# Kernel tuning notes

Measured on AMD Instinct MI355X. Metric: run time of the kernel, lower is better.

Reference implementation:

```python
import jax, jax.numpy as jnp
import numpy as np

N_NODES = 100000


def setup_inputs() -> dict:
    key = jax.random.key(0)
    ks = jax.random.split(key, 10)
    N, T, IN, H, OUT = N_NODES, 20, 1, 64, 1
    E = 3200000
    s = 1.0 / np.sqrt(H)
    return {
        "x": jax.random.normal(ks[0], (N, T, IN), dtype=jnp.float32),
        "edge_index": jax.random.randint(ks[1], (E, 2), 0, N, dtype=jnp.int64),
        "W_ih": jax.random.uniform(ks[2], (H, IN), jnp.float32, -s, s),
        "b_ih": jax.random.uniform(ks[3], (H,), jnp.float32, -s, s),
        "W_hh": jax.random.uniform(ks[4], (H, H), jnp.float32, -s, s),
        "b_hh": jax.random.uniform(ks[5], (H,), jnp.float32, -s, s),
        "W_gcn": jax.random.uniform(ks[6], (H, H), jnp.float32, -s, s),
        "b_gcn": jax.random.uniform(ks[7], (H,), jnp.float32, -s, s),
        "W_fc": jax.random.uniform(ks[8], (OUT, H), jnp.float32, -s, s),
        "b_fc": jax.random.uniform(ks[9], (OUT,), jnp.float32, -s, s),
    }


def _strnn_fwd(x, edge_index, W_ih, b_ih, W_hh, b_hh, W_gcn, b_gcn, W_fc, b_fc):
    N = x.shape[0]
    H = W_hh.shape[0]

    # ---- vanilla tanh RNN (batch_first); only last hidden state is needed ----
    xs = jnp.swapaxes(x, 0, 1)  # [T, N, in]

    def step(h, xt):
        h = jnp.tanh(xt @ W_ih.T + b_ih + h @ W_hh.T + b_hh)
        return h, None

    h_last, _ = jax.lax.scan(step, jnp.zeros((N, H), x.dtype), xs)  # [N, H]

    # ---- GCNConv: add self-loops, sym-normalize, linear, scatter-add ----
    src = edge_index[:, 0]
    dst = edge_index[:, 1]
    loop = jnp.arange(N, dtype=src.dtype)
    src = jnp.concatenate([src, loop])
    dst = jnp.concatenate([dst, loop])

    xw = h_last @ W_gcn.T  # [N, H]
    deg = jax.ops.segment_sum(jnp.ones_like(dst, dtype=xw.dtype), dst, num_segments=N)
    dinv = jnp.where(deg > 0, jax.lax.rsqrt(deg), 0.0)
    norm = dinv[src] * dinv[dst]  # [E+N]

    msgs = xw[src] * norm[:, None]  # gather + scale, [E+N, H]
    agg = jax.ops.segment_sum(msgs, dst, num_segments=N) + b_gcn  # scatter-add

    return agg @ W_fc.T + b_fc  # [N, out]


def reference(x, edge_index, W_ih, b_ih, W_hh, b_hh, W_gcn, b_gcn, W_fc, b_fc):
    return _strnn_fwd(x, edge_index, W_ih, b_ih, W_hh, b_hh, W_gcn, b_gcn, W_fc, b_fc)
```

## Files before the change

kernel.cpp:

```cpp
#include <hip/hip_runtime.h>

#define TT 20
#define HH 64
#define RSZ 32768
#define DRSZ 16384
#define NSL 64
#define NSLD 32

typedef __attribute__((ext_vector_type(8))) short short8;
typedef __attribute__((ext_vector_type(4))) float f32x4;

__device__ __forceinline__ unsigned fbits(float f) { union { float f; unsigned u; } v; v.f = f; return v.u; }
__device__ __forceinline__ float bcast(unsigned u) { union { float f; unsigned u; } v; v.u = u; return v.f; }

__global__ __launch_bounds__(256, 3) void k_fused(
    const float* __restrict__ x,
    const float* __restrict__ W_ih, const float* __restrict__ b_ih,
    const float* __restrict__ W_hh, const float* __restrict__ b_hh,
    const float* __restrict__ W_gcn, const float* __restrict__ W_fc,
    const int* __restrict__ ei, unsigned* __restrict__ degrep,
    float* __restrict__ z, int N, int E, int RD, int N2)
{
    __shared__ __align__(16) unsigned smem[8192];

    const int t = threadIdx.x;
    const int RDN = RD * NSLD;

    if (blockIdx.x < RDN) {
        unsigned* bin = smem;
        const int r = blockIdx.x % RD;
        const int s = blockIdx.x / RD;
        const int base = r * DRSZ;
        for (int i = t; i < DRSZ / 2; i += 256) bin[i] = 0;
        __syncthreads();
        const long long P = (long long)(E >> 1);
        const long long pb = s * P / NSLD;
        const long long pe = (s + 1) * P / NSLD;
        const int4* ei4 = (const int4*)ei;
        for (long long g = pb + t; g < pe; g += 256) {
            int4 q = ei4[g];
            unsigned u0 = (unsigned)(q.y - base);
            unsigned u1 = (unsigned)(q.w - base);
            if (u0 < DRSZ) atomicAdd(&bin[u0 >> 1], 1u << ((u0 & 1) << 4));
            if (u1 < DRSZ) atomicAdd(&bin[u1 >> 1], 1u << ((u1 & 1) << 4));
        }
        if ((E & 1) && s == NSLD - 1 && t == 0) {
            unsigned u = (unsigned)(ei[2 * (E - 1) + 1] - base);
            if (u < DRSZ) atomicAdd(&bin[u >> 1], 1u << ((u & 1) << 4));
        }
        __syncthreads();
        const int lim = min(DRSZ, N - base);
        const int words = (lim + 1) >> 1;
        unsigned* dst = degrep + (size_t)s * N2 + (base >> 1);
        for (int i = t; i < words; i += 256) dst[i] = bin[i];
        return;
    }

    const int w    = t >> 6;
    const int l    = t & 63;
    const int nl   = l & 15;
    const int quad = l >> 4;
    const int n0   = (blockIdx.x - RDN) * 64 + w * 16;

    unsigned short* hh = (unsigned short*)&smem[w * 512];
    unsigned short* hl = (unsigned short*)&smem[2048 + w * 512];
    float*          sx = (float*)&smem[4096 + w * 320];

    for (int i = l; i < 16 * TT; i += 64) {
        int nn = i / TT, tt = i - nn * TT;
        int n = n0 + nn; if (n >= N) n = N - 1;
        sx[tt * 16 + nn] = x[(size_t)n * TT + tt];
    }
    {
        uint4 zz = {0, 0, 0, 0};
        uint4* ph = (uint4*)hh;
        uint4* pl = (uint4*)hl;
#pragma unroll
        for (int i = 0; i < 2; ++i) { ph[l + 64 * i] = zz; pl[l + 64 * i] = zz; }
    }

    short8 Bh[4][2], Bl[4][2];
#pragma unroll
    for (int tt2 = 0; tt2 < 4; ++tt2)
#pragma unroll
        for (int kc = 0; kc < 2; ++kc) {
            const float* wr = W_hh + (size_t)(16 * tt2 + nl) * HH + kc * 32 + quad * 8;
            float4 w0 = *(const float4*)(wr);
            float4 w1 = *(const float4*)(wr + 4);
            float wvv[8] = {w0.x, w0.y, w0.z, w0.w, w1.x, w1.y, w1.z, w1.w};
            short8 sh, sl;
#pragma unroll
            for (int j = 0; j < 8; ++j) {
                unsigned u  = fbits(wvv[j]);
                unsigned hb = u & 0xffff0000u;
                float lo = wvv[j] - bcast(hb);
                sh[j] = (short)(hb >> 16);
                sl[j] = (short)(fbits(lo) >> 16);
            }
            Bh[tt2][kc] = sh; Bl[tt2][kc] = sl;
        }

    float vl = 0.0f;
#pragma unroll 8
    for (int j = 0; j < HH; ++j) vl = fmaf(W_fc[j], W_gcn[j * HH + l], vl);

    float wih4[4], bs4[4], vv[4];
#pragma unroll
    for (int tt2 = 0; tt2 < 4; ++tt2) {
        int n = nl + 16 * tt2;
        wih4[tt2] = W_ih[n];
        bs4[tt2]  = b_ih[n] + b_hh[n];
        vv[tt2]   = __shfl(vl, n, 64);
    }

    const int ra = (l ^ ((l >> 4) & 1)) * 8;

    f32x4 C[4];

    for (int step = 0; step < TT; ++step) {
        const float4 xr = *(const float4*)&sx[step * 16 + quad * 4];
#pragma unroll
        for (int tt2 = 0; tt2 < 4; ++tt2) {
            C[tt2][0] = fmaf(xr.x, wih4[tt2], bs4[tt2]);
            C[tt2][1] = fmaf(xr.y, wih4[tt2], bs4[tt2]);
            C[tt2][2] = fmaf(xr.z, wih4[tt2], bs4[tt2]);
            C[tt2][3] = fmaf(xr.w, wih4[tt2], bs4[tt2]);
        }

#pragma unroll
        for (int kc = 0; kc < 2; ++kc) {
            short8 Ah = *(const short8*)&hh[kc * 512 + ra];
            short8 Al = *(const short8*)&hl[kc * 512 + ra];
#pragma unroll
            for (int tt2 = 0; tt2 < 4; ++tt2) {
                C[tt2] = __builtin_amdgcn_mfma_f32_16x16x32_bf16(Ah, Bh[tt2][kc], C[tt2], 0, 0, 0);
                C[tt2] = __builtin_amdgcn_mfma_f32_16x16x32_bf16(Ah, Bl[tt2][kc], C[tt2], 0, 0, 0);
                C[tt2] = __builtin_amdgcn_mfma_f32_16x16x32_bf16(Al, Bh[tt2][kc], C[tt2], 0, 0, 0);
            }
        }

#pragma unroll
        for (int tt2 = 0; tt2 < 4; ++tt2) {
            const int kc_d = tt2 >> 1;
            const int qa   = (nl >> 3) + 2 * (tt2 & 1);
            const int jj   = nl & 7;
#pragma unroll
            for (int r = 0; r < 4; ++r) {
                float eg = __builtin_amdgcn_exp2f(C[tt2][r] * 2.885390081777927f);
                float hv = fmaf(-2.0f, __builtin_amdgcn_rcpf(eg + 1.0f), 1.0f);
                C[tt2][r] = hv;
                unsigned um = fbits(hv);
                unsigned hb = um & 0xffff0000u;
                float lo = hv - bcast(hb);
                const int m   = quad * 4 + r;
                const int la  = m + 16 * qa;
                const int idx = kc_d * 512 + (la ^ ((la >> 4) & 1)) * 8 + jj;
                hh[idx] = (unsigned short)(um >> 16);
                hl[idx] = (unsigned short)(fbits(lo) >> 16);
            }
        }
    }

#pragma unroll
    for (int r = 0; r < 4; ++r) {
        float p = 0.0f;
#pragma unroll
        for (int tt2 = 0; tt2 < 4; ++tt2) p = fmaf(C[tt2][r], vv[tt2], p);
        p += __shfl_xor(p, 1, 64);
        p += __shfl_xor(p, 2, 64);
        p += __shfl_xor(p, 4, 64);
        p += __shfl_xor(p, 8, 64);
        if (nl == 0) {
            const int n = n0 + quad * 4 + r;
            if (n < N) z[n] = p;
        }
    }
}

__global__ __launch_bounds__(256) void k_w(const unsigned* __restrict__ degrep,
                                           const float* __restrict__ z,
                                           float* __restrict__ dinv,
                                           float* __restrict__ w, int N, int N2) {
    int n = blockIdx.x * blockDim.x + threadIdx.x;
    if (n >= N) return;
    const int wd = n >> 1, sh = (n & 1) << 4;
    unsigned d = 0;
#pragma unroll 8
    for (int s = 0; s < NSLD; ++s) d += (degrep[(size_t)s * N2 + wd] >> sh) & 0xffffu;
    float di = __frsqrt_rn((float)d + 1.0f);
    dinv[n] = di;
    w[n] = di * z[n];
}

__global__ __launch_bounds__(1024) void k_edge_bin(const int* __restrict__ ei,
                                                   const float* __restrict__ w,
                                                   float* __restrict__ Srep,
                                                   int N, int E, int R) {
    extern __shared__ float bin[];
    const int r = blockIdx.x % R;
    const int s = blockIdx.x / R;
    const int base = r * RSZ;
    for (int i = threadIdx.x; i < RSZ; i += 1024) bin[i] = 0.0f;
    __syncthreads();
    const long long P = (long long)(E >> 1);
    const long long pb = s * P / NSL;
    const long long pe = (s + 1) * P / NSL;
    const int4* ei4 = (const int4*)ei;
    for (long long g = pb + threadIdx.x; g < pe; g += 1024) {
        int4 q = ei4[g];
        unsigned u0 = (unsigned)(q.y - base);
        unsigned u1 = (unsigned)(q.w - base);
        if (u0 < RSZ) atomicAdd(&bin[u0], w[q.x]);
        if (u1 < RSZ) atomicAdd(&bin[u1], w[q.z]);
    }
    if ((E & 1) && s == NSL - 1 && threadIdx.x == 0) {
        unsigned u = (unsigned)(ei[2 * (E - 1) + 1] - base);
        if (u < RSZ) atomicAdd(&bin[u], w[ei[2 * (E - 1)]]);
    }
    __syncthreads();
    const int lim = min(RSZ, N - base);
    float* dst = Srep + (size_t)s * N + base;
    for (int i = threadIdx.x; i < lim; i += 1024) dst[i] = bin[i];
}

__global__ __launch_bounds__(256) void k_final(const float* __restrict__ dinv,
                                               const float* __restrict__ Srep,
                                               const float* __restrict__ w,
                                               const float* __restrict__ b_gcn,
                                               const float* __restrict__ W_fc,
                                               const float* __restrict__ b_fc,
                                               float* __restrict__ out, int N)
{
    float c = b_fc[0];
#pragma unroll 8
    for (int j = 0; j < HH; ++j) c = fmaf(W_fc[j], b_gcn[j], c);
    int n = blockIdx.x * blockDim.x + threadIdx.x;
    if (n >= N) return;
    float S = 0.0f;
#pragma unroll 8
    for (int s = 0; s < NSL; ++s) S += Srep[(size_t)s * N + n];
    float d = dinv[n];
    out[n] = fmaf(d, S, fmaf(d, w[n], c));
}

extern "C" void kernel_launch(void* const* d_in, const int* in_sizes, int n_in,
                              void* d_out, int out_size, void* d_ws, size_t ws_size,
                              hipStream_t stream)
{
    const float* x     = (const float*)d_in[0];
    const int*   ei    = (const int*)d_in[1];
    const float* W_ih  = (const float*)d_in[2];
    const float* b_ih  = (const float*)d_in[3];
    const float* W_hh  = (const float*)d_in[4];
    const float* b_hh  = (const float*)d_in[5];
    const float* W_gcn = (const float*)d_in[6];
    const float* b_gcn = (const float*)d_in[7];
    const float* W_fc  = (const float*)d_in[8];
    const float* b_fc  = (const float*)d_in[9];
    float* out = (float*)d_out;

    const int N  = in_sizes[0] / TT;
    const int E  = in_sizes[1] / 2;
    const int N2 = (N + 1) / 2;
    const int RD = (N + DRSZ - 1) / DRSZ;
    const int RS = (N + RSZ - 1) / RSZ;

    static bool s_attr = false;
    if (!s_attr) {
        hipFuncSetAttribute((const void*)k_edge_bin,
                            hipFuncAttributeMaxDynamicSharedMemorySize, RSZ * 4);
        s_attr = true;
    }

    char* ws = (char*)d_ws;
    size_t off = 0;
    auto alloc = [&](size_t bytes) { void* p = ws + off; off += (bytes + 255) & ~(size_t)255; return p; };
    unsigned* degrep = (unsigned*)alloc((size_t)NSLD * N2 * 4);
    float*    Srep   = (float*)   alloc((size_t)NSL * N * 4);
    float*    z      = (float*)   alloc((size_t)N * 4);
    float*    dinv   = (float*)   alloc((size_t)N * 4);
    float*    w      = (float*)   alloc((size_t)N * 4);

    const int rnnBlocks = (N + 63) / 64;
    k_fused   <<<RD * NSLD + rnnBlocks, 256, 0, stream>>>(x, W_ih, b_ih, W_hh, b_hh,
                                                          W_gcn, W_fc, ei, degrep,
                                                          z, N, E, RD, N2);
    k_w       <<<(N + 255) / 256, 256, 0, stream>>>(degrep, z, dinv, w, N, N2);
    k_edge_bin<<<RS * NSL, 1024, RSZ * 4, stream>>>(ei, w, Srep, N, E, RS);
    k_final   <<<(N + 255) / 256, 256, 0, stream>>>(dinv, Srep, w, b_gcn, W_fc, b_fc, out, N);
}
```

Measured before the change: 216.1 us.

## Replace LDS-binned degree replicas with direct global atomics on degree array

The degree count no longer uses per-range LDS bins with packed 16-bit counters written to replicated slices. Each of 64 edge-slice blocks now does 32-bit atomicAdd straight into a single global degree array, cleared by a memset. This removes the repeated edge scans across node ranges (the old code read all edges RD times) and the replica reduction in k_w. The fused kernel's LDS shrinks and occupancy rises to 6 blocks per CU. The cost is about 3.2M global atomics to random addresses, plus an extra memset launch.

```diff
diff --git a/kernel.cpp b/kernel.cpp
--- a/kernel.cpp
+++ b/kernel.cpp
@@ -3,9 +3,8 @@
 #define TT 20
 #define HH 64
 #define RSZ 32768
-#define DRSZ 16384
 #define NSL 64
-#define NSLD 32
+#define NSLD 64
 
 typedef __attribute__((ext_vector_type(8))) short short8;
 typedef __attribute__((ext_vector_type(4))) float f32x4;
@@ -13,46 +12,31 @@
 __device__ __forceinline__ unsigned fbits(float f) { union { float f; unsigned u; } v; v.f = f; return v.u; }
 __device__ __forceinline__ float bcast(unsigned u) { union { float f; unsigned u; } v; v.u = u; return v.f; }
 
-__global__ __launch_bounds__(256, 3) void k_fused(
+__global__ __launch_bounds__(256, 6) void k_fused(
     const float* __restrict__ x,
     const float* __restrict__ W_ih, const float* __restrict__ b_ih,
     const float* __restrict__ W_hh, const float* __restrict__ b_hh,
     const float* __restrict__ W_gcn, const float* __restrict__ W_fc,
-    const int* __restrict__ ei, unsigned* __restrict__ degrep,
-    float* __restrict__ z, int N, int E, int RD, int N2)
+    const int* __restrict__ ei, unsigned* __restrict__ deg,
+    float* __restrict__ z, int N, int E)
 {
-    __shared__ __align__(16) unsigned smem[8192];
+    __shared__ __align__(16) unsigned smem[5376];
 
     const int t = threadIdx.x;
-    const int RDN = RD * NSLD;
-
-    if (blockIdx.x < RDN) {
-        unsigned* bin = smem;
-        const int r = blockIdx.x % RD;
-        const int s = blockIdx.x / RD;
-        const int base = r * DRSZ;
-        for (int i = t; i < DRSZ / 2; i += 256) bin[i] = 0;
-        __syncthreads();
+
+    if (blockIdx.x < NSLD) {
+        const int s = blockIdx.x;
         const long long P = (long long)(E >> 1);
         const long long pb = s * P / NSLD;
         const long long pe = (s + 1) * P / NSLD;
         const int4* ei4 = (const int4*)ei;
         for (long long g = pb + t; g < pe; g += 256) {
             int4 q = ei4[g];
-            unsigned u0 = (unsigned)(q.y - base);
-            unsigned u1 = (unsigned)(q.w - base);
-            if (u0 < DRSZ) atomicAdd(&bin[u0 >> 1], 1u << ((u0 & 1) << 4));
-            if (u1 < DRSZ) atomicAdd(&bin[u1 >> 1], 1u << ((u1 & 1) << 4));
-        }
-        if ((E & 1) && s == NSLD - 1 && t == 0) {
-            unsigned u = (unsigned)(ei[2 * (E - 1) + 1] - base);
-            if (u < DRSZ) atomicAdd(&bin[u >> 1], 1u << ((u & 1) << 4));
-        }
-        __syncthreads();
-        const int lim = min(DRSZ, N - base);
-        const int words = (lim + 1) >> 1;
-        unsigned* dst = degrep + (size_t)s * N2 + (base >> 1);
-        for (int i = t; i < words; i += 256) dst[i] = bin[i];
+            atomicAdd(&deg[q.y], 1u);
+            atomicAdd(&deg[q.w], 1u);
+        }
+        if ((E & 1) && s == NSLD - 1 && t == 0)
+            atomicAdd(&deg[ei[2 * (E - 1) + 1]], 1u);
         return;
     }
 
@@ -60,7 +44,7 @@
     const int l    = t & 63;
     const int nl   = l & 15;
     const int quad = l >> 4;
-    const int n0   = (blockIdx.x - RDN) * 64 + w * 16;
+    const int n0   = (blockIdx.x - NSLD) * 64 + w * 16;
 
     unsigned short* hh = (unsigned short*)&smem[w * 512];
     unsigned short* hl = (unsigned short*)&smem[2048 + w * 512];
@@ -177,17 +161,13 @@
     }
 }
 
-__global__ __launch_bounds__(256) void k_w(const unsigned* __restrict__ degrep,
+__global__ __launch_bounds__(256) void k_w(const unsigned* __restrict__ deg,
                                            const float* __restrict__ z,
                                            float* __restrict__ dinv,
-                                           float* __restrict__ w, int N, int N2) {
+                                           float* __restrict__ w, int N) {
     int n = blockIdx.x * blockDim.x + threadIdx.x;
     if (n >= N) return;
-    const int wd = n >> 1, sh = (n & 1) << 4;
-    unsigned d = 0;
-#pragma unroll 8
-    for (int s = 0; s < NSLD; ++s) d += (degrep[(size_t)s * N2 + wd] >> sh) & 0xffffu;
-    float di = __frsqrt_rn((float)d + 1.0f);
+    float di = __frsqrt_rn((float)deg[n] + 1.0f);
     dinv[n] = di;
     w[n] = di * z[n];
 }
@@ -261,8 +241,6 @@
 
     const int N  = in_sizes[0] / TT;
     const int E  = in_sizes[1] / 2;
-    const int N2 = (N + 1) / 2;
-    const int RD = (N + DRSZ - 1) / DRSZ;
     const int RS = (N + RSZ - 1) / RSZ;
 
     static bool s_attr = false;
@@ -275,17 +253,18 @@
     char* ws = (char*)d_ws;
     size_t off = 0;
     auto alloc = [&](size_t bytes) { void* p = ws + off; off += (bytes + 255) & ~(size_t)255; return p; };
-    unsigned* degrep = (unsigned*)alloc((size_t)NSLD * N2 * 4);
-    float*    Srep   = (float*)   alloc((size_t)NSL * N * 4);
-    float*    z      = (float*)   alloc((size_t)N * 4);
-    float*    dinv   = (float*)   alloc((size_t)N * 4);
-    float*    w      = (float*)   alloc((size_t)N * 4);
+    unsigned* deg  = (unsigned*)alloc((size_t)N * 4);
+    float*    Srep = (float*)   alloc((size_t)NSL * N * 4);
+    float*    z    = (float*)   alloc((size_t)N * 4);
+    float*    dinv = (float*)   alloc((size_t)N * 4);
+    float*    w    = (float*)   alloc((size_t)N * 4);
+
+    hipMemsetAsync(deg, 0, (size_t)N * 4, stream);
 
     const int rnnBlocks = (N + 63) / 64;
-    k_fused   <<<RD * NSLD + rnnBlocks, 256, 0, stream>>>(x, W_ih, b_ih, W_hh, b_hh,
-                                                          W_gcn, W_fc, ei, degrep,
-                                                          z, N, E, RD, N2);
-    k_w       <<<(N + 255) / 256, 256, 0, stream>>>(degrep, z, dinv, w, N, N2);
+    k_fused   <<<NSLD + rnnBlocks, 256, 0, stream>>>(x, W_ih, b_ih, W_hh, b_hh,
+                                                     W_gcn, W_fc, ei, deg, z, N, E);
+    k_w       <<<(N + 255) / 256, 256, 0, stream>>>(deg, z, dinv, w, N);
     k_edge_bin<<<RS * NSL, 1024, RSZ * 4, stream>>>(ei, w, Srep, N, E, RS);
     k_final   <<<(N + 255) / 256, 256, 0, stream>>>(dinv, Srep, w, b_gcn, W_fc, b_fc, out, N);
 }
```

Measured after the change: 544.7 us. +152.1%, slower.
